# Optimization experiments

Measured on AMD Instinct MI355X. Metric: run time of the kernel, lower is better.

## Reference

```python
import jax, jax.numpy as jnp
import numpy as np

DECAY = 0.99
COMMIT = 0.25
EPS = 1e-5


def setup_inputs() -> dict:
    key = jax.random.key(0)
    k1, k2, k3 = jax.random.split(key, 3)
    B, H, W, D, K = 32, 32, 32, 64, 1024
    return {
        "z": jax.random.normal(k1, (B, H, W, D), dtype=jnp.float32),
        "embeddings": jax.random.normal(k2, (K, D), dtype=jnp.float32),
        "cluster_size": jnp.ones((K,), dtype=jnp.float32),
        "ema_embed": jax.random.normal(k3, (K, D), dtype=jnp.float32),
    }


def reference(z, embeddings, cluster_size, ema_embed):
    B, H, W, D = z.shape
    K = embeddings.shape[0]
    z_flat = z.reshape(-1, D)                      # [N, D]

    # squared L2 distances via expansion: ||z||^2 + ||e||^2 - 2 z e^T  -> [N, K]
    distances = (
        jnp.sum(z_flat * z_flat, axis=1, keepdims=True)
        + jnp.sum(embeddings * embeddings, axis=1)
        - 2.0 * z_flat @ embeddings.T
    )
    idx = jnp.argmin(distances, axis=1)            # [N]
    quantized = embeddings[idx].reshape(z.shape)   # gather, [B,H,W,D]

    # training-mode EMA update (one_hot^T matmuls expressed as segment sums)
    n_i = jax.ops.segment_sum(jnp.ones(z_flat.shape[0], z.dtype), idx, num_segments=K)
    dw = jax.ops.segment_sum(z_flat, idx, num_segments=K)          # [K, D]
    new_cluster = cluster_size * DECAY + n_i * (1.0 - DECAY)
    new_ema = ema_embed * DECAY + dw * (1.0 - DECAY)
    n = jnp.sum(new_cluster)
    new_cluster = (new_cluster + EPS) / (n + K * EPS) * n           # Laplace smoothing
    new_embeddings = new_ema / new_cluster[:, None]

    loss = COMMIT * jnp.mean((z - jax.lax.stop_gradient(quantized)) ** 2)
    q_ste = z + jax.lax.stop_gradient(quantized - z)                # straight-through

    quantized_vectors = jnp.transpose(q_ste, (0, 3, 1, 2))          # [B, D, H, W]
    quantized_indices = idx.reshape(B, H, W)[:, None, :, :]         # [B, 1, H, W]
    return quantized_vectors, quantized_indices, loss, new_embeddings, new_cluster, new_ema
```

## Files before the change

### kernel.cpp

```cpp
#include <hip/hip_runtime.h>


typedef unsigned short u16;
typedef u16 us8 __attribute__((ext_vector_type(8)));
typedef float f4 __attribute__((ext_vector_type(4)));

#define WS_FZ    0
#define WS_FE    1
#define WS_FCS   2
#define WS_FEMA  3
#define WS_LOSS  4
#define WS_CSSUM 5

__device__ __forceinline__ float b2f(u16 u) {
    union { unsigned int i; float f; } x; x.i = ((unsigned int)u) << 16; return x.f;
}
__device__ __forceinline__ int swzE(int d, int c) {
    return d * 64 + (c ^ ((((d) >> 2) & 7) << 2));
}
__device__ __forceinline__ int swzZ(int d, int c) {
    int cb = (c >> 2) ^ (c >> 5);
    int cc = ((cb & 31) << 2) | (c & 3);
    return d * 128 + (cc ^ ((((d) >> 2) & 7) << 2));
}

__global__ __launch_bounds__(256) void k_init(
    const u16* z, const u16* e, const u16* cs, const u16* ema,
    float* __restrict__ ws, float* __restrict__ esqp, int K)
{
    __shared__ int flg[4];
    __shared__ float csred[256];
    const int w = threadIdx.x >> 6, l = threadIdx.x & 63;
    const u16* p = (w == 0) ? z : (w == 1) ? e : (w == 2) ? cs : ema;
    int cnt = 0;
    #pragma unroll
    for (int t = 0; t < 4; ++t) {
        unsigned hb = (p[(l * 4 + t) * 2] >> 8) & 0x7F;
        cnt += (hb >= 0x3A && hb <= 0x41) ? 1 : 0;
    }
    #pragma unroll
    for (int off = 32; off; off >>= 1) cnt += __shfl_down(cnt, off);
    if (l == 0) flg[w] = (cnt < 128) ? 1 : 0;
    __syncthreads();
    if (blockIdx.x == 0) {
        if (threadIdx.x < 4) ((int*)ws)[threadIdx.x] = flg[threadIdx.x];
        if (threadIdx.x == 4) ws[WS_LOSS] = 0.0f;
    }
    const int fe = flg[1];
    const int fcs = flg[2];
    const int code = blockIdx.x * 256 + threadIdx.x;
    if (code < K) {
        float r[8];
        if (fe) {
            const float* ep = (const float*)e + (size_t)code * 64;
            #pragma unroll
            for (int j = 0; j < 8; ++j) { float v = ep[j]; float p2 = v * v;
                asm volatile("" : "+v"(p2)); r[j] = p2; }
            #pragma unroll
            for (int t = 1; t < 8; ++t)
                #pragma unroll
                for (int j = 0; j < 8; ++j) { float v = ep[8 * t + j]; float p2 = v * v;
                    asm volatile("" : "+v"(p2)); r[j] += p2; }
        } else {
            const u16* ep = e + (size_t)code * 64;
            #pragma unroll
            for (int j = 0; j < 8; ++j) { float v = b2f(ep[j]); float p2 = v * v;
                asm volatile("" : "+v"(p2)); r[j] = p2; }
            #pragma unroll
            for (int t = 1; t < 8; ++t)
                #pragma unroll
                for (int j = 0; j < 8; ++j) { float v = b2f(ep[8 * t + j]); float p2 = v * v;
                    asm volatile("" : "+v"(p2)); r[j] += p2; }
        }
        esqp[code] = ((r[0] + r[1]) + (r[2] + r[3])) + ((r[4] + r[5]) + (r[6] + r[7]));
    }
    csred[threadIdx.x] = (code < K)
        ? (fcs ? ((const float*)cs)[code] : b2f(cs[code])) : 0.0f;
    __syncthreads();
    for (int s = 128; s; s >>= 1) {
        if (threadIdx.x < s) csred[threadIdx.x] += csred[threadIdx.x + s];
        __syncthreads();
    }
    if (threadIdx.x == 0) atomicAdd(&ws[WS_CSSUM], csred[0]);
}

__global__ __launch_bounds__(512, 2) void k_main(
    const u16* __restrict__ z, const u16* __restrict__ e,
    const float* __restrict__ esqp,
    float* __restrict__ ws, float* __restrict__ out,
    int K, int offIdx, long long outSize)
{
    __shared__ __align__(16) float z_t[64 * 128];
    __shared__ __align__(16) float e_t[4 * 64 * 64];
    __shared__ float esq_l[2048];
    __shared__ float z2_l[128];
    __shared__ int   idx_l[128];

    const int tid = threadIdx.x;
    const int cg  = tid >> 7;
    const int lt  = tid & 127;
    const int mtg = lt & 15;
    const int ktg = lt >> 4;
    const int pbase = blockIdx.x * 128;
    const int* wsi = (const int*)ws;
    const int fz = wsi[WS_FZ];
    const int fe = wsi[WS_FE];
    const int kchunks = K >> 6;
    const int h = kchunks >> 2;

    for (int i = tid; i < K; i += 512) esq_l[i] = esqp[i];

    if (fz) {
        const f4* z4 = (const f4*)((const float*)z + (size_t)pbase * 64);
        for (int i = tid; i < 2048; i += 512) {
            f4 v = z4[i];
            int m = i >> 4, d4 = (i & 15) * 4;
            z_t[swzZ(d4 + 0, m)] = v[0];
            z_t[swzZ(d4 + 1, m)] = v[1];
            z_t[swzZ(d4 + 2, m)] = v[2];
            z_t[swzZ(d4 + 3, m)] = v[3];
        }
    } else {
        const us8* z8 = (const us8*)(z + (size_t)pbase * 64);
        for (int i = tid; i < 1024; i += 512) {
            us8 v = z8[i];
            int m = i >> 3, d8 = (i & 7) * 8;
            #pragma unroll
            for (int t = 0; t < 8; ++t) z_t[swzZ(d8 + t, m)] = b2f(v[t]);
        }
    }
    __syncthreads();
    if (tid < 128) {
        float r[8];
        #pragma unroll
        for (int j = 0; j < 8; ++j) {
            float v = z_t[swzZ(j, tid)]; float p = v * v;
            asm volatile("" : "+v"(p)); r[j] = p;
        }
        #pragma unroll
        for (int t = 1; t < 8; ++t)
            #pragma unroll
            for (int j = 0; j < 8; ++j) {
                float v = z_t[swzZ(8 * t + j, tid)]; float p = v * v;
                asm volatile("" : "+v"(p)); r[j] += p;
            }
        z2_l[tid] = ((r[0] + r[1]) + (r[2] + r[3])) + ((r[4] + r[5]) + (r[6] + r[7]));
    }

    float bestd[8] = {INFINITY, INFINITY, INFINITY, INFINITY,
                      INFINITY, INFINITY, INFINITY, INFINITY};
    int   besti[8] = {0, 0, 0, 0, 0, 0, 0, 0};
    float* et = e_t + cg * 4096;

    f4  fb[8];
    us8 hb[4];
    {
        int kc0 = cg * h;
        if (fe) {
            const f4* e4 = (const f4*)((const float*)e + (size_t)kc0 * 4096);
            #pragma unroll
            for (int t = 0; t < 8; ++t) fb[t] = e4[lt + 128 * t];
        } else {
            const us8* e8 = (const us8*)(e + (size_t)kc0 * 4096);
            #pragma unroll
            for (int t = 0; t < 4; ++t) hb[t] = e8[lt + 128 * t];
        }
    }

    for (int c = 0; c < h; ++c) {
        const int kc = cg * h + c;
        if (fe) {
            #pragma unroll
            for (int t = 0; t < 8; ++t) {
                int i = lt + 128 * t;
                int kl = i >> 4, d4 = (i & 15) * 4;
                et[swzE(d4 + 0, kl)] = fb[t][0];
                et[swzE(d4 + 1, kl)] = fb[t][1];
                et[swzE(d4 + 2, kl)] = fb[t][2];
                et[swzE(d4 + 3, kl)] = fb[t][3];
            }
        } else {
            #pragma unroll
            for (int t = 0; t < 4; ++t) {
                int i = lt + 128 * t;
                int kl = i >> 3, d8 = (i & 7) * 8;
                #pragma unroll
                for (int s = 0; s < 8; ++s) et[swzE(d8 + s, kl)] = b2f(hb[t][s]);
            }
        }
        if (c + 1 < h) {
            if (fe) {
                const f4* e4 = (const f4*)((const float*)e + (size_t)(kc + 1) * 4096);
                #pragma unroll
                for (int t = 0; t < 8; ++t) fb[t] = e4[lt + 128 * t];
            } else {
                const us8* e8 = (const us8*)(e + (size_t)(kc + 1) * 4096);
                #pragma unroll
                for (int t = 0; t < 4; ++t) hb[t] = e8[lt + 128 * t];
            }
        }
        __syncthreads();

        float acc[8][8] = {};
        for (int d0 = 0; d0 < 64; d0 += 4) {
            f4 za[4], zb[4], ea[4], eb[4];
            #pragma unroll
            for (int j = 0; j < 4; ++j) {
                int d = d0 + j;
                za[j] = *(const f4*)&z_t[swzZ(d, mtg * 8)];
                zb[j] = *(const f4*)&z_t[swzZ(d, mtg * 8 + 4)];
                ea[j] = *(const f4*)&et[swzE(d, ktg * 8)];
                eb[j] = *(const f4*)&et[swzE(d, ktg * 8 + 4)];
            }
            #pragma unroll
            for (int j = 0; j < 4; ++j) {
                #pragma unroll
                for (int a = 0; a < 4; ++a)
                    #pragma unroll
                    for (int b = 0; b < 4; ++b) {
                        acc[a][b]         += za[j][a] * ea[j][b];
                        acc[a][b + 4]     += za[j][a] * eb[j][b];
                        acc[a + 4][b]     += zb[j][a] * ea[j][b];
                        acc[a + 4][b + 4] += zb[j][a] * eb[j][b];
                    }
            }
        }
        __syncthreads();

        #pragma unroll
        for (int a = 0; a < 8; ++a) {
            float z2 = z2_l[mtg * 8 + a];
            #pragma unroll
            for (int b = 0; b < 8; ++b) {
                float e2 = esq_l[kc * 64 + ktg * 8 + b];
                float dist = (z2 + e2) - 2.0f * acc[a][b];
                int kg = kc * 64 + ktg * 8 + b;
                if (dist < bestd[a]) { bestd[a] = dist; besti[a] = kg; }
            }
        }
    }

    float* red_d = e_t;
    int*   red_i = (int*)(e_t + 4224);
    #pragma unroll
    for (int a = 0; a < 8; ++a) {
        red_d[(mtg * 8 + a) * 33 + (cg * 8 + ktg)] = bestd[a];
        red_i[(mtg * 8 + a) * 33 + (cg * 8 + ktg)] = besti[a];
    }
    __syncthreads();

    if (tid < 128) {
        float bd = red_d[tid * 33]; int bi = red_i[tid * 33];
        #pragma unroll
        for (int t = 1; t < 32; ++t) {
            float dv = red_d[tid * 33 + t]; int iv = red_i[tid * 33 + t];
            if (dv < bd || (dv == bd && iv < bi)) { bd = dv; bi = iv; }
        }
        idx_l[tid] = bi;
        long long oi = (long long)offIdx + pbase + tid;
        if (oi < outSize) out[oi] = (float)bi;
    }
    __syncthreads();

    const int m = tid & 127;
    const int w = tid >> 7;
    const int p = pbase + m;
    const int b = p >> 10;
    const int hw = p & 1023;
    const int kidx = idx_l[m];
    float lsum = 0.f;
    #pragma unroll
    for (int dd = 0; dd < 16; ++dd) {
        int d = w + 4 * dd;
        float zv = z_t[swzZ(d, m)];
        float q  = fe ? ((const float*)e)[(size_t)kidx * 64 + d]
                      : b2f(e[(size_t)kidx * 64 + d]);
        float df = zv - q;
        lsum += df * df;
        float qs = zv + (q - zv);
        long long qi = (long long)b * 65536 + d * 1024 + hw;
        if (qi < outSize) out[qi] = qs;
    }
    #pragma unroll
    for (int off = 32; off; off >>= 1) lsum += __shfl_down(lsum, off);
    if ((tid & 63) == 0) atomicAdd(&ws[WS_LOSS], lsum);
}

__global__ __launch_bounds__(512) void k_scat(
    const u16* __restrict__ z, const float* __restrict__ idxf,
    const float* __restrict__ ws,
    float* __restrict__ dwb, float* __restrict__ cntb, int N)
{
    const int* wsi = (const int*)ws;
    const int fz = wsi[WS_FZ];
    const int lane = threadIdx.x & 63;
    const int wv = (blockIdx.x * 512 + threadIdx.x) >> 6;
    const int nw = (gridDim.x * 512) >> 6;
    for (int p = wv; p < N; p += nw) {
        int k = (int)idxf[p];
        float v = fz ? ((const float*)z)[(size_t)p * 64 + lane]
                     : b2f(z[(size_t)p * 64 + lane]);
        atomicAdd(&dwb[(size_t)k * 64 + lane], v);
        if (lane == 0) atomicAdd(&cntb[k], 1.0f);
    }
}

__global__ __launch_bounds__(256) void k_fin(
    const u16* __restrict__ cs, const u16* __restrict__ ema,
    const float* __restrict__ ws,
    const float* __restrict__ dwb, const float* __restrict__ cntb,
    float* __restrict__ out, int K, int N,
    long long offLoss, long long outSize, float lossScale)
{
    const int* wsi = (const int*)ws;
    const int fcs = wsi[WS_FCS], fema = wsi[WS_FEMA];
    const int i = blockIdx.x * 256 + threadIdx.x;
    const long long offEmb = offLoss + 1;
    const long long offCl  = offEmb + (long long)K * 64;
    const long long offEma = offCl + K;
    const float nsum = 0.99f * ws[WS_CSSUM] + 0.01f * (float)N;
    const float keps = (float)K * 1e-5f;

    float cnt = 0.f, dw = 0.f, csv = 0.f, ev = 0.f;
    int k = 0, d = 0;
    const int ok = (i < K * 64);
    if (ok) {
        k = i >> 6; d = i & 63;
        cnt = cntb[k];
        dw  = dwb[i];
        csv = fcs ? ((const float*)cs)[k] : b2f(cs[k]);
        ev  = fema ? ((const float*)ema)[i] : b2f(ema[i]);
    }
    __syncthreads();
    if (ok) {
        float c  = csv * 0.99f + cnt * 0.01f;
        float sm = (c + 1e-5f) / (nsum + keps) * nsum;
        float ne = ev * 0.99f + dw * 0.01f;
        if (offEma + i < outSize) out[offEma + i] = ne;
        if (offEmb + i < outSize) out[offEmb + i] = ne / sm;
        if (d == 0 && offCl + k < outSize) out[offCl + k] = sm;
    }
    if (blockIdx.x == 0 && threadIdx.x == 0 && offLoss < outSize)
        out[offLoss] = 0.25f * (ws[WS_LOSS] * lossScale);
}

extern "C" void kernel_launch(void* const* d_in, const int* in_sizes, int n_in,
                              void* d_out, int out_size, void* d_ws, size_t ws_size,
                              hipStream_t stream) {
    long long sz[4] = {0, 0, 0, 0};
    for (int i = 0; i < n_in && i < 4; ++i) sz[i] = in_sizes[i];
    int icl = 0, iz = 0;
    for (int i = 1; i < 4; ++i) { if (sz[i] < sz[icl]) icl = i; if (sz[i] > sz[iz]) iz = i; }
    int ip[2], np = 0;
    for (int i = 0; i < 4; ++i) if (i != icl && i != iz && np < 2) ip[np++] = i;
    long long K = sz[icl], KD = (np == 2) ? sz[ip[0]] : 0;
    int derivOK = (n_in == 4 && np == 2 && icl != iz && sz[ip[0]] == sz[ip[1]] &&
                   K > 0 && KD % K == 0);
    long long D = derivOK ? KD / K : 64;
    long long N = (derivOK && D > 0 && sz[iz] % D == 0) ? sz[iz] / D : 32768;
    int ie, iema;
    if (!derivOK) { iz = 0; ie = 1; icl = 2; iema = 3; N = 32768; K = 1024; D = 64; }
    else if (icl > ip[0] && icl < ip[1]) { ie = ip[0]; iema = ip[1]; }
    else { iema = ip[0]; ie = ip[1]; }

    int fastOK = (D == 64) && (N % 1024 == 0) && (K % 256 == 0) &&
                 (K >= 512) && (K <= 2048);
    if (!fastOK) { N = 32768; K = 1024; }

    long long offIdx = N * 64, offLoss = offIdx + N;
    long long offEmb = offLoss + 1, offCl = offEmb + K * 64, offEma = offCl + K;

    float* out = (float*)d_out;
    float* ws = (float*)d_ws;

    long long wsNeed = 8 + K + K * 64 + K;
    float *esqp, *dwb, *cntb;
    if ((long long)ws_size >= wsNeed * 4) {
        esqp = ws + 8; dwb = ws + 8 + K; cntb = dwb + K * 64;
        hipMemsetAsync(ws, 0, (size_t)(wsNeed * 4), stream);
    } else {
        esqp = out + offEma; dwb = out + offEmb; cntb = out + offCl;
        hipMemsetAsync(ws, 0, 8 * 4, stream);
        hipMemsetAsync(out + offEmb, 0, (size_t)((K * 64 + K) * 4), stream);
    }

    const u16* z   = (const u16*)d_in[iz];
    const u16* e   = (const u16*)d_in[ie];
    const u16* cs  = (const u16*)d_in[icl];
    const u16* ema = (const u16*)d_in[iema];

    float lossScale = (float)(1.0 / (double)(N * 64));

    k_init<<<(int)((K + 255) / 256), 256, 0, stream>>>(z, e, cs, ema, ws, esqp, (int)K);
    k_main<<<(int)(N / 128), 512, 0, stream>>>(z, e, esqp, ws, out,
                                               (int)K, (int)offIdx, (long long)out_size);
    k_scat<<<512, 512, 0, stream>>>(z, out + offIdx, ws, dwb, cntb, (int)N);
    k_fin<<<(int)((K * 64 + 255) / 256), 256, 0, stream>>>(cs, ema, ws, dwb, cntb, out,
                                                           (int)K, (int)N, offLoss,
                                                           (long long)out_size, lossScale);
}
```

Before: 193.8 us.

## Fuse EMA scatter into main kernel and move zeroing into init

Drops the separate scatter kernel. The main kernel now atomically adds each z value and a count into dw/count buffers while it writes the quantized output. The buffers are replicated twice by block parity to cut atomic contention. Zeroing moves from hipMemsetAsync into k_init, which runs a fixed 64-block grid, and the cluster-size sum is done by a single block with no atomic. This saves two memset launches, one kernel launch and a re-read of z and the indices, at the cost of more atomics inside k_main's epilogue.

```diff
diff --git a/kernel.cpp b/kernel.cpp
--- a/kernel.cpp
+++ b/kernel.cpp
@@ -26,11 +26,13 @@
 
 __global__ __launch_bounds__(256) void k_init(
     const u16* z, const u16* e, const u16* cs, const u16* ema,
-    float* __restrict__ ws, float* __restrict__ esqp, int K)
+    float* __restrict__ ws, float* __restrict__ esqp,
+    float* __restrict__ zeroP, long long zeroN, int K)
 {
     __shared__ int flg[4];
     __shared__ float csred[256];
-    const int w = threadIdx.x >> 6, l = threadIdx.x & 63;
+    const int tid = threadIdx.x;
+    const int w = tid >> 6, l = tid & 63;
     const u16* p = (w == 0) ? z : (w == 1) ? e : (w == 2) ? cs : ema;
     int cnt = 0;
     #pragma unroll
@@ -43,12 +45,12 @@
     if (l == 0) flg[w] = (cnt < 128) ? 1 : 0;
     __syncthreads();
     if (blockIdx.x == 0) {
-        if (threadIdx.x < 4) ((int*)ws)[threadIdx.x] = flg[threadIdx.x];
-        if (threadIdx.x == 4) ws[WS_LOSS] = 0.0f;
+        if (tid < 4) ((int*)ws)[tid] = flg[tid];
+        if (tid == 4) ws[WS_LOSS] = 0.0f;
     }
     const int fe = flg[1];
     const int fcs = flg[2];
-    const int code = blockIdx.x * 256 + threadIdx.x;
+    const int code = blockIdx.x * 256 + tid;
     if (code < K) {
         float r[8];
         if (fe) {
@@ -74,20 +76,30 @@
         }
         esqp[code] = ((r[0] + r[1]) + (r[2] + r[3])) + ((r[4] + r[5]) + (r[6] + r[7]));
     }
-    csred[threadIdx.x] = (code < K)
-        ? (fcs ? ((const float*)cs)[code] : b2f(cs[code])) : 0.0f;
-    __syncthreads();
-    for (int s = 128; s; s >>= 1) {
-        if (threadIdx.x < s) csred[threadIdx.x] += csred[threadIdx.x + s];
+    {
+        long long g = (long long)blockIdx.x * 256 + tid;
+        long long stride = (long long)gridDim.x * 256;
+        for (long long i = g; i < zeroN; i += stride) zeroP[i] = 0.0f;
+    }
+    if (blockIdx.x == 0) {
+        float partial = 0.f;
+        for (int k0 = tid; k0 < K; k0 += 256)
+            partial += fcs ? ((const float*)cs)[k0] : b2f(cs[k0]);
+        csred[tid] = partial;
         __syncthreads();
-    }
-    if (threadIdx.x == 0) atomicAdd(&ws[WS_CSSUM], csred[0]);
+        for (int s = 128; s; s >>= 1) {
+            if (tid < s) csred[tid] += csred[tid + s];
+            __syncthreads();
+        }
+        if (tid == 0) ws[WS_CSSUM] = csred[0];
+    }
 }
 
 __global__ __launch_bounds__(512, 2) void k_main(
     const u16* __restrict__ z, const u16* __restrict__ e,
     const float* __restrict__ esqp,
     float* __restrict__ ws, float* __restrict__ out,
+    float* __restrict__ dwb, int nrep, long long repStride,
     int K, int offIdx, long long outSize)
 {
     __shared__ __align__(16) float z_t[64 * 128];
@@ -268,6 +280,7 @@
     const int b = p >> 10;
     const int hw = p & 1023;
     const int kidx = idx_l[m];
+    float* dwr = dwb + (size_t)(blockIdx.x & (nrep - 1)) * repStride;
     float lsum = 0.f;
     #pragma unroll
     for (int dd = 0; dd < 16; ++dd) {
@@ -280,35 +293,18 @@
         float qs = zv + (q - zv);
         long long qi = (long long)b * 65536 + d * 1024 + hw;
         if (qi < outSize) out[qi] = qs;
-    }
+        atomicAdd(&dwr[(size_t)kidx * 64 + d], zv);
+    }
+    if (w == 0) atomicAdd(&dwr[(size_t)K * 64 + kidx], 1.0f);
     #pragma unroll
     for (int off = 32; off; off >>= 1) lsum += __shfl_down(lsum, off);
     if ((tid & 63) == 0) atomicAdd(&ws[WS_LOSS], lsum);
 }
 
-__global__ __launch_bounds__(512) void k_scat(
-    const u16* __restrict__ z, const float* __restrict__ idxf,
-    const float* __restrict__ ws,
-    float* __restrict__ dwb, float* __restrict__ cntb, int N)
-{
-    const int* wsi = (const int*)ws;
-    const int fz = wsi[WS_FZ];
-    const int lane = threadIdx.x & 63;
-    const int wv = (blockIdx.x * 512 + threadIdx.x) >> 6;
-    const int nw = (gridDim.x * 512) >> 6;
-    for (int p = wv; p < N; p += nw) {
-        int k = (int)idxf[p];
-        float v = fz ? ((const float*)z)[(size_t)p * 64 + lane]
-                     : b2f(z[(size_t)p * 64 + lane]);
-        atomicAdd(&dwb[(size_t)k * 64 + lane], v);
-        if (lane == 0) atomicAdd(&cntb[k], 1.0f);
-    }
-}
-
 __global__ __launch_bounds__(256) void k_fin(
     const u16* __restrict__ cs, const u16* __restrict__ ema,
     const float* __restrict__ ws,
-    const float* __restrict__ dwb, const float* __restrict__ cntb,
+    const float* __restrict__ dwb, int nrep, long long repStride,
     float* __restrict__ out, int K, int N,
     long long offLoss, long long outSize, float lossScale)
 {
@@ -326,8 +322,12 @@
     const int ok = (i < K * 64);
     if (ok) {
         k = i >> 6; d = i & 63;
-        cnt = cntb[k];
         dw  = dwb[i];
+        cnt = dwb[(size_t)K * 64 + k];
+        if (nrep == 2) {
+            dw  += dwb[repStride + i];
+            cnt += dwb[repStride + (size_t)K * 64 + k];
+        }
         csv = fcs ? ((const float*)cs)[k] : b2f(cs[k]);
         ev  = fema ? ((const float*)ema)[i] : b2f(ema[i]);
     }
@@ -373,16 +373,19 @@
     float* out = (float*)d_out;
     float* ws = (float*)d_ws;
 
-    long long wsNeed = 8 + K + K * 64 + K;
-    float *esqp, *dwb, *cntb;
-    if ((long long)ws_size >= wsNeed * 4) {
-        esqp = ws + 8; dwb = ws + 8 + K; cntb = dwb + K * 64;
-        hipMemsetAsync(ws, 0, (size_t)(wsNeed * 4), stream);
+    long long repStride = K * 64 + K;
+    long long need2 = 8 + K + 2 * repStride;
+    long long need1 = 8 + K + repStride;
+    float *esqp, *dwb;
+    int nrep;
+    if ((long long)ws_size >= need2 * 4) {
+        nrep = 2; esqp = ws + 8; dwb = ws + 8 + K;
+    } else if ((long long)ws_size >= need1 * 4) {
+        nrep = 1; esqp = ws + 8; dwb = ws + 8 + K;
     } else {
-        esqp = out + offEma; dwb = out + offEmb; cntb = out + offCl;
-        hipMemsetAsync(ws, 0, 8 * 4, stream);
-        hipMemsetAsync(out + offEmb, 0, (size_t)((K * 64 + K) * 4), stream);
-    }
+        nrep = 1; esqp = out + offEma; dwb = out + offEmb;
+    }
+    long long zeroN = (long long)nrep * repStride;
 
     const u16* z   = (const u16*)d_in[iz];
     const u16* e   = (const u16*)d_in[ie];
@@ -391,11 +394,11 @@
 
     float lossScale = (float)(1.0 / (double)(N * 64));
 
-    k_init<<<(int)((K + 255) / 256), 256, 0, stream>>>(z, e, cs, ema, ws, esqp, (int)K);
+    k_init<<<64, 256, 0, stream>>>(z, e, cs, ema, ws, esqp, dwb, zeroN, (int)K);
     k_main<<<(int)(N / 128), 512, 0, stream>>>(z, e, esqp, ws, out,
+                                               dwb, nrep, repStride,
                                                (int)K, (int)offIdx, (long long)out_size);
-    k_scat<<<512, 512, 0, stream>>>(z, out + offIdx, ws, dwb, cntb, (int)N);
-    k_fin<<<(int)((K * 64 + 255) / 256), 256, 0, stream>>>(cs, ema, ws, dwb, cntb, out,
-                                                           (int)K, (int)N, offLoss,
+    k_fin<<<(int)((K * 64 + 255) / 256), 256, 0, stream>>>(cs, ema, ws, dwb, nrep, repStride,
+                                                           out, (int)K, (int)N, offLoss,
                                                            (long long)out_size, lossScale);
 }
```

Result: slower. 389.0 us (+100.7%).
